# Optimization experiments

Measured on AMD Instinct MI355X. Metric: run time of the kernel, lower is better.

The kernel has to match this reference:

```python
import jax, jax.numpy as jnp
import numpy as np

B, LP, NC, D, E = 8, 1000, 64, 128, 320  # batch, protein len, compound atoms, hid dim, esm dim


def _linear_params(key, din, dout):
    k1, k2 = jax.random.split(key)
    lim = 1.0 / np.sqrt(din)
    W = jax.random.uniform(k1, (din, dout), minval=-lim, maxval=lim, dtype=jnp.float32)
    b = jax.random.uniform(k2, (dout,), minval=-lim, maxval=lim, dtype=jnp.float32)
    return W, b


def setup_inputs() -> dict:
    key = jax.random.key(0)
    ks = jax.random.split(key, 14)
    inp = {
        "protein_embedding": jax.random.normal(ks[0], (B, LP, E), dtype=jnp.float32),
        "protein_feat_x": jax.random.normal(ks[1], (B, LP, D), dtype=jnp.float32),
        "compound_feats": jax.random.normal(ks[2], (B, NC, D), dtype=jnp.float32),
    }
    layers = [("emb", E, D), ("wq", D, D), ("wk", D, D), ("wv", D, D), ("wo", D, D),
              ("jp", D, D), ("jc", D, D),
              ("c1", D, 1024), ("c2", 1024, 1024), ("c3", 1024, 256), ("c4", 256, 1)]
    for i, (name, din, dout) in enumerate(layers):
        W, b = _linear_params(ks[3 + i], din, dout)
        inp[name + "_w"] = W
        inp[name + "_b"] = b
    return inp


def reference(protein_embedding, protein_feat_x, compound_feats,
              emb_w, emb_b, wq_w, wq_b, wk_w, wk_b, wv_w, wv_b, wo_w, wo_b,
              jp_w, jp_b, jc_w, jc_b,
              c1_w, c1_b, c2_w, c2_b, c3_w, c3_b, c4_w, c4_b):
    # protein sequence embedding -> hid dim
    pe = protein_embedding @ emb_w + emb_b                      # [B, LP, D]
    # single-head cross attention: query = seq embedding, key/value = graph feats
    Q = pe @ wq_w + wq_b
    K = protein_feat_x @ wk_w + wk_b
    V = protein_feat_x @ wv_w + wv_b
    scale = jnp.sqrt(jnp.asarray(D, pe.dtype))                  # n_heads=1 -> head_dim=D
    attn = jax.nn.softmax(jnp.einsum('bqd,bkd->bqk', Q, K) / scale, axis=-1)
    protein_feats = jnp.einsum('bqk,bkd->bqd', attn, V) @ wo_w + wo_b  # [B, LP, D]

    # sigmoid bilinear joint attention over (protein residue, compound atom) pairs
    P = jax.nn.relu(protein_feats) @ jp_w + jp_b                # [B, LP, D]
    C = jax.nn.relu(compound_feats) @ jc_w + jc_b               # [B, NC, D]
    A = jax.nn.sigmoid(jnp.einsum('bid,bkd->bik', P, C))        # [B, LP, NC]
    A = A / jnp.sum(A, axis=(1, 2), keepdims=True)

    # tanh outer product (the costly 4D bikj intermediate) then weighted reduction
    cp = jnp.tanh(protein_feats[:, :, None, :] * compound_feats[:, None, :, :])  # [B, LP, NC, D]
    cp_embedding = jnp.einsum('bikd,bik->bd', cp, A)            # [B, D]

    # classifier MLP (dropout is eval-mode identity)
    h = jax.nn.relu(cp_embedding @ c1_w + c1_b)
    h = jax.nn.relu(h @ c2_w + c2_b)
    h = jax.nn.relu(h @ c3_w + c3_b)
    return h @ c4_w + c4_b                                      # [B, 1]
```

## Files before the change

### kernel.cpp

```cpp
#include <hip/hip_runtime.h>
#include <hip/hip_bf16.h>
#include <math.h>

#define LP 1000
#define NCMP 64
#define NSPLIT 4

typedef _Float16 f16;
typedef f16   v8h __attribute__((ext_vector_type(8)));
typedef float v4f __attribute__((ext_vector_type(4)));

__device__ __forceinline__ float rcp_fast(float x) { return __builtin_amdgcn_rcpf(x); }
__device__ __forceinline__ void fsplit(float x, f16& h, f16& l) {
    h = (f16)x; l = (f16)(x - (float)h);
}

__device__ __forceinline__ void gemm_core(float (*Ws)[128], float (*Xt)[36],
                                          const float* X, const float* W, const float* bias,
                                          float* Y, int K, int rowbase, bool relu_in)
{
    const int t  = threadIdx.x;
    const int r0 = (t >> 5) * 4;
    const int c0 = (t & 31) * 4;
    const int xr = t >> 3, xk = (t & 7) << 2;
    const int xrow = rowbase + xr;
    float4 xv = *(const float4*)(X + (long)xrow * K + xk);
    float4 wv[4];
    #pragma unroll
    for (int u = 0; u < 4; ++u) {
        int s = t + u * 256, r = s >> 5, cb = (s & 31) << 2;
        wv[u] = *(const float4*)(W + (long)r * 128 + cb);
    }
    float acc[4][4] = {};
    for (int k0 = 0; k0 < K; k0 += 32) {
        float4 xs = xv;
        if (relu_in) { xs.x = fmaxf(xs.x,0.f); xs.y = fmaxf(xs.y,0.f);
                       xs.z = fmaxf(xs.z,0.f); xs.w = fmaxf(xs.w,0.f); }
        Xt[xk+0][xr] = xs.x; Xt[xk+1][xr] = xs.y; Xt[xk+2][xr] = xs.z; Xt[xk+3][xr] = xs.w;
        #pragma unroll
        for (int u = 0; u < 4; ++u) {
            int s = t + u * 256, r = s >> 5, cb = (s & 31) << 2;
            *(float4*)&Ws[r][cb] = wv[u];
        }
        __syncthreads();
        if (k0 + 32 < K) {
            xv = *(const float4*)(X + (long)xrow * K + k0 + 32 + xk);
            #pragma unroll
            for (int u = 0; u < 4; ++u) {
                int s = t + u * 256, r = s >> 5, cb = (s & 31) << 2;
                wv[u] = *(const float4*)(W + (long)(k0 + 32 + r) * 128 + cb);
            }
        }
        #pragma unroll
        for (int kk = 0; kk < 32; ++kk) {
            float4 w4 = *(const float4*)&Ws[kk][c0];
            float4 x4 = *(const float4*)&Xt[kk][r0];
            acc[0][0] = fmaf(x4.x, w4.x, acc[0][0]); acc[0][1] = fmaf(x4.x, w4.y, acc[0][1]);
            acc[0][2] = fmaf(x4.x, w4.z, acc[0][2]); acc[0][3] = fmaf(x4.x, w4.w, acc[0][3]);
            acc[1][0] = fmaf(x4.y, w4.x, acc[1][0]); acc[1][1] = fmaf(x4.y, w4.y, acc[1][1]);
            acc[1][2] = fmaf(x4.y, w4.z, acc[1][2]); acc[1][3] = fmaf(x4.y, w4.w, acc[1][3]);
            acc[2][0] = fmaf(x4.z, w4.x, acc[2][0]); acc[2][1] = fmaf(x4.z, w4.y, acc[2][1]);
            acc[2][2] = fmaf(x4.z, w4.z, acc[2][2]); acc[2][3] = fmaf(x4.z, w4.w, acc[2][3]);
            acc[3][0] = fmaf(x4.w, w4.x, acc[3][0]); acc[3][1] = fmaf(x4.w, w4.y, acc[3][1]);
            acc[3][2] = fmaf(x4.w, w4.z, acc[3][2]); acc[3][3] = fmaf(x4.w, w4.w, acc[3][3]);
        }
        __syncthreads();
    }
    float4 bv = bias ? *(const float4*)(bias + c0) : make_float4(0.f,0.f,0.f,0.f);
    #pragma unroll
    for (int i = 0; i < 4; ++i) {
        int row = rowbase + r0 + i;
        float4 o;
        o.x = acc[i][0] + bv.x; o.y = acc[i][1] + bv.y;
        o.z = acc[i][2] + bv.z; o.w = acc[i][3] + bv.w;
        *(float4*)(Y + (long)row * 128 + c0) = o;
    }
}

struct H4 { f16 a, b, c, d; };

__device__ __forceinline__ void gemm_core16(float (*Ws)[128], float (*Xt)[36],
                                            const float* X, const float* W, const float* bias,
                                            f16* Yhi, f16* Ylo, int K, int rowbase)
{
    const int t  = threadIdx.x;
    const int r0 = (t >> 5) * 4;
    const int c0 = (t & 31) * 4;
    const int xr = t >> 3, xk = (t & 7) << 2;
    const int xrow = rowbase + xr;
    float4 xv = *(const float4*)(X + (long)xrow * K + xk);
    float4 wv[4];
    #pragma unroll
    for (int u = 0; u < 4; ++u) {
        int s = t + u * 256, r = s >> 5, cb = (s & 31) << 2;
        wv[u] = *(const float4*)(W + (long)r * 128 + cb);
    }
    float acc[4][4] = {};
    for (int k0 = 0; k0 < K; k0 += 32) {
        Xt[xk+0][xr] = xv.x; Xt[xk+1][xr] = xv.y; Xt[xk+2][xr] = xv.z; Xt[xk+3][xr] = xv.w;
        #pragma unroll
        for (int u = 0; u < 4; ++u) {
            int s = t + u * 256, r = s >> 5, cb = (s & 31) << 2;
            *(float4*)&Ws[r][cb] = wv[u];
        }
        __syncthreads();
        if (k0 + 32 < K) {
            xv = *(const float4*)(X + (long)xrow * K + k0 + 32 + xk);
            #pragma unroll
            for (int u = 0; u < 4; ++u) {
                int s = t + u * 256, r = s >> 5, cb = (s & 31) << 2;
                wv[u] = *(const float4*)(W + (long)(k0 + 32 + r) * 128 + cb);
            }
        }
        #pragma unroll
        for (int kk = 0; kk < 32; ++kk) {
            float4 w4 = *(const float4*)&Ws[kk][c0];
            float4 x4 = *(const float4*)&Xt[kk][r0];
            acc[0][0] = fmaf(x4.x, w4.x, acc[0][0]); acc[0][1] = fmaf(x4.x, w4.y, acc[0][1]);
            acc[0][2] = fmaf(x4.x, w4.z, acc[0][2]); acc[0][3] = fmaf(x4.x, w4.w, acc[0][3]);
            acc[1][0] = fmaf(x4.y, w4.x, acc[1][0]); acc[1][1] = fmaf(x4.y, w4.y, acc[1][1]);
            acc[1][2] = fmaf(x4.y, w4.z, acc[1][2]); acc[1][3] = fmaf(x4.y, w4.w, acc[1][3]);
            acc[2][0] = fmaf(x4.z, w4.x, acc[2][0]); acc[2][1] = fmaf(x4.z, w4.y, acc[2][1]);
            acc[2][2] = fmaf(x4.z, w4.z, acc[2][2]); acc[2][3] = fmaf(x4.z, w4.w, acc[2][3]);
            acc[3][0] = fmaf(x4.w, w4.x, acc[3][0]); acc[3][1] = fmaf(x4.w, w4.y, acc[3][1]);
            acc[3][2] = fmaf(x4.w, w4.z, acc[3][2]); acc[3][3] = fmaf(x4.w, w4.w, acc[3][3]);
        }
        __syncthreads();
    }
    float4 bv = *(const float4*)(bias + c0);
    #pragma unroll
    for (int i = 0; i < 4; ++i) {
        int row = rowbase + r0 + i;
        int bb = row / 1000, rr = row - bb * 1000;
        long base = ((long)bb * 1024 + rr) * 128 + c0;
        float o0 = acc[i][0]+bv.x, o1 = acc[i][1]+bv.y, o2 = acc[i][2]+bv.z, o3 = acc[i][3]+bv.w;
        H4 h, l;
        fsplit(o0, h.a, l.a); fsplit(o1, h.b, l.b); fsplit(o2, h.c, l.c); fsplit(o3, h.d, l.d);
        *(H4*)(Yhi + base) = h;
        *(H4*)(Ylo + base) = l;
    }
}

__global__ __launch_bounds__(256) void pre0_k(const float* __restrict__ emb_w, const float* __restrict__ emb_b,
                                              const float* __restrict__ wq_w, const float* __restrict__ wq_b,
                                              const float* __restrict__ wv_w, const float* __restrict__ wv_b,
                                              const float* __restrict__ wo_w, const float* __restrict__ wo_b,
                                              float* __restrict__ Wp, float* __restrict__ bp,
                                              float* __restrict__ Wvo, float* __restrict__ bvo,
                                              float* __restrict__ zbase)
{
    __shared__ __align__(16) float Ws[32][128];
    __shared__ __align__(16) float Xt[32][36];
    const int bid = blockIdx.x;
    if (bid < 10) { gemm_core(Ws, Xt, emb_w, wq_w, nullptr, Wp, 128, bid * 32, false); return; }
    if (bid >= 11 && bid < 15) { gemm_core(Ws, Xt, wv_w, wo_w, nullptr, Wvo, 128, (bid - 11) * 32, false); return; }
    int t = threadIdx.x;
    if (bid == 10 && t >= 128) {
        for (int i = t - 128; i < 1032; i += 128) zbase[i] = 0.f;
        return;
    }
    if (t < 128) {
        const float* vb = (bid == 10) ? emb_b : wv_b;
        const float* Wm = (bid == 10) ? wq_w  : wo_w;
        const float* ab = (bid == 10) ? wq_b  : wo_b;
        float a0 = 0.f, a1 = 0.f, a2 = 0.f, a3 = 0.f;
        for (int k = 0; k < 128; k += 4) {
            a0 = fmaf(vb[k+0], Wm[(k+0)*128 + t], a0);
            a1 = fmaf(vb[k+1], Wm[(k+1)*128 + t], a1);
            a2 = fmaf(vb[k+2], Wm[(k+2)*128 + t], a2);
            a3 = fmaf(vb[k+3], Wm[(k+3)*128 + t], a3);
        }
        float* dst = (bid == 10) ? bp : bvo;
        dst[t] = (a0 + a1) + (a2 + a3) + ab[t];
    }
}

__global__ __launch_bounds__(256) void qkv_k(const float* __restrict__ PE, const float* __restrict__ Wp,
                                             const float* __restrict__ bp, const float* __restrict__ PFX,
                                             const float* __restrict__ wk_w, const float* __restrict__ wk_b,
                                             const float* __restrict__ CF, const float* __restrict__ jc_w,
                                             const float* __restrict__ jc_b,
                                             f16* __restrict__ Qhi, f16* __restrict__ Qlo,
                                             f16* __restrict__ Khi, f16* __restrict__ Klo,
                                             f16* __restrict__ Vthi, f16* __restrict__ Vtlo,
                                             float* __restrict__ Cj)
{
    __shared__ __align__(16) float Ws[32][128];
    __shared__ __align__(16) float Xt[32][36];
    const int bid = blockIdx.x;
    if (bid < 250) { gemm_core16(Ws, Xt, PE, Wp, bp, Qhi, Qlo, 320, bid * 32); return; }
    if (bid < 500) { gemm_core16(Ws, Xt, PFX, wk_w, wk_b, Khi, Klo, 128, (bid - 250) * 32); return; }
    if (bid < 516) { gemm_core(Ws, Xt, CF, jc_w, jc_b, Cj, 128, (bid - 500) * 32, true); return; }
    const int t = threadIdx.x;
    const int rowbase = (bid - 516) * 32;
    const int d = t >> 1, half = t & 1;
    #pragma unroll 4
    for (int i = 0; i < 16; ++i) {
        int row = rowbase + half * 16 + i;
        int bb = row / 1000, rr = row - bb * 1000;
        float v = PFX[(long)row * 128 + d];
        f16 h, l; fsplit(v, h, l);
        long o = ((long)bb * 128 + d) * 1024 + rr;
        Vthi[o] = h; Vtlo[o] = l;
    }
}

__global__ __launch_bounds__(256) void flash7_k(const f16* __restrict__ Qhi, const f16* __restrict__ Qlo,
                                                const f16* __restrict__ Khi, const f16* __restrict__ Klo,
                                                const f16* __restrict__ Vthi, const f16* __restrict__ Vtlo,
                                                float* __restrict__ Opart,
                                                float* __restrict__ mpart, float* __restrict__ lpart)
{
    __shared__ __align__(16) f16 KVhi[9216];
    __shared__ __align__(16) f16 KVlo[9216];
    __shared__ __align__(16) f16 Pshi[4][16 * 72];
    __shared__ __align__(16) f16 Pslo[4][16 * 72];
    const int t    = threadIdx.x;
    const int wv   = t >> 6;
    const int lane = t & 63;
    const int quad = lane >> 4;
    const int l4   = lane & 15;
    const int qt = blockIdx.x, sp = blockIdx.y, b = blockIdx.z;
    const int q0 = qt * 64;
    const float SCALE = 0.08838834764831845f;
    const float L2E   = 1.4426950408889634f;

    int qrow = q0 + wv * 16 + l4; if (qrow >= LP) qrow = LP - 1;
    const long qbase = ((long)b * 1024 + qrow) * 128;
    v8h qh[4], ql[4];
    #pragma unroll
    for (int kt4 = 0; kt4 < 4; ++kt4) {
        qh[kt4] = *(const v8h*)(Qhi + qbase + kt4 * 32 + quad * 8);
        ql[kt4] = *(const v8h*)(Qlo + qbase + kt4 * 32 + quad * 8);
    }
    float m_i[4] = { -3.0e38f, -3.0e38f, -3.0e38f, -3.0e38f };
    float l_i[4] = { 0.f, 0.f, 0.f, 0.f };
    v4f  O[8];
    #pragma unroll
    for (int dt = 0; dt < 8; ++dt) O[dt] = (v4f){0.f, 0.f, 0.f, 0.f};

    for (int kt = sp * 4; kt < sp * 4 + 4; ++kt) {
        const int key0 = kt * 64;
        __syncthreads();
        #pragma unroll
        for (int u = 0; u < 4; ++u) {
            int ch = t + u * 256;
            int r = ch >> 4, co = (ch & 15) * 8;
            long ga = ((long)b * 1024 + key0 + r) * 128 + co;
            *(v8h*)(KVhi + r * 136 + co) = *(const v8h*)(Khi + ga);
            *(v8h*)(KVlo + r * 136 + co) = *(const v8h*)(Klo + ga);
        }
        __syncthreads();
        v8h vh[4], vl[4];
        #pragma unroll
        for (int u = 0; u < 4; ++u) {
            int ch = t + u * 256;
            int d = ch >> 3, co = (ch & 7) * 8;
            long ga = ((long)b * 128 + d) * 1024 + key0 + co;
            vh[u] = *(const v8h*)(Vthi + ga);
            vl[u] = *(const v8h*)(Vtlo + ga);
        }
        v4f S[4];
        #pragma unroll
        for (int nt = 0; nt < 4; ++nt) S[nt] = (v4f){0.f, 0.f, 0.f, 0.f};
        #pragma unroll
        for (int nt = 0; nt < 4; ++nt) {
            const int rb = (nt * 16 + l4) * 136;
            #pragma unroll
            for (int kt4 = 0; kt4 < 4; ++kt4) {
                v8h bh = *(const v8h*)(KVhi + rb + kt4 * 32 + quad * 8);
                v8h bl = *(const v8h*)(KVlo + rb + kt4 * 32 + quad * 8);
                S[nt] = __builtin_amdgcn_mfma_f32_16x16x32_f16(qh[kt4], bh, S[nt], 0, 0, 0);
                S[nt] = __builtin_amdgcn_mfma_f32_16x16x32_f16(qh[kt4], bl, S[nt], 0, 0, 0);
                S[nt] = __builtin_amdgcn_mfma_f32_16x16x32_f16(ql[kt4], bh, S[nt], 0, 0, 0);
            }
        }
        #pragma unroll
        for (int nt = 0; nt < 4; ++nt) {
            bool valid = (key0 + nt * 16 + l4) < LP;
            #pragma unroll
            for (int r = 0; r < 4; ++r)
                S[nt][r] = valid ? S[nt][r] * SCALE : -3.0e38f;
        }
        float alpha[4];
        #pragma unroll
        for (int r = 0; r < 4; ++r) {
            float tm = fmaxf(fmaxf(S[0][r], S[1][r]), fmaxf(S[2][r], S[3][r]));
            tm = fmaxf(tm, __shfl_xor(tm, 1));
            tm = fmaxf(tm, __shfl_xor(tm, 2));
            tm = fmaxf(tm, __shfl_xor(tm, 4));
            tm = fmaxf(tm, __shfl_xor(tm, 8));
            float mnew = fmaxf(m_i[r], tm);
            alpha[r] = exp2f((m_i[r] - mnew) * L2E);
            float ps = 0.f;
            #pragma unroll
            for (int nt = 0; nt < 4; ++nt) {
                float p = exp2f((S[nt][r] - mnew) * L2E);
                S[nt][r] = p;
                ps += p;
            }
            ps += __shfl_xor(ps, 1);
            ps += __shfl_xor(ps, 2);
            ps += __shfl_xor(ps, 4);
            ps += __shfl_xor(ps, 8);
            l_i[r] = l_i[r] * alpha[r] + ps;
            m_i[r] = mnew;
        }
        #pragma unroll
        for (int dt = 0; dt < 8; ++dt) {
            O[dt][0] *= alpha[0]; O[dt][1] *= alpha[1];
            O[dt][2] *= alpha[2]; O[dt][3] *= alpha[3];
        }
        __syncthreads();
        #pragma unroll
        for (int u = 0; u < 4; ++u) {
            int ch = t + u * 256;
            int d = ch >> 3, co = (ch & 7) * 8;
            *(v8h*)(KVhi + d * 72 + co) = vh[u];
            *(v8h*)(KVlo + d * 72 + co) = vl[u];
        }
        #pragma unroll
        for (int nt = 0; nt < 4; ++nt) {
            int col = nt * 16 + l4;
            #pragma unroll
            for (int r = 0; r < 4; ++r) {
                f16 ph, pl; fsplit(S[nt][r], ph, pl);
                Pshi[wv][(quad * 4 + r) * 72 + col] = ph;
                Pslo[wv][(quad * 4 + r) * 72 + col] = pl;
            }
        }
        __syncthreads();
        #pragma unroll
        for (int kc = 0; kc < 2; ++kc) {
            v8h pah = *(const v8h*)(Pshi[wv] + l4 * 72 + kc * 32 + quad * 8);
            v8h pal = *(const v8h*)(Pslo[wv] + l4 * 72 + kc * 32 + quad * 8);
            #pragma unroll
            for (int dt = 0; dt < 8; ++dt) {
                v8h vfh = *(const v8h*)(KVhi + (dt * 16 + l4) * 72 + kc * 32 + quad * 8);
                v8h vfl = *(const v8h*)(KVlo + (dt * 16 + l4) * 72 + kc * 32 + quad * 8);
                O[dt] = __builtin_amdgcn_mfma_f32_16x16x32_f16(pah, vfh, O[dt], 0, 0, 0);
                O[dt] = __builtin_amdgcn_mfma_f32_16x16x32_f16(pah, vfl, O[dt], 0, 0, 0);
                O[dt] = __builtin_amdgcn_mfma_f32_16x16x32_f16(pal, vfh, O[dt], 0, 0, 0);
            }
        }
    }
    #pragma unroll
    for (int r = 0; r < 4; ++r) {
        int row = q0 + wv * 16 + quad * 4 + r;
        if (row < LP) {
            long base = (long)sp * 1024000 + ((long)b * LP + row) * 128;
            #pragma unroll
            for (int dt = 0; dt < 8; ++dt)
                Opart[base + dt * 16 + l4] = O[dt][r];
            if (l4 == 0) {
                mpart[(long)sp * 8000 + b * LP + row] = m_i[r];
                lpart[(long)sp * 8000 + b * LP + row] = l_i[r];
            }
        }
    }
}

__global__ __launch_bounds__(256) void mt1a_k(
    const float* __restrict__ Opart, const float* __restrict__ mp, const float* __restrict__ lp,
    const float* __restrict__ Wvo, const float* __restrict__ bvo, float* __restrict__ PF)
{
    __shared__ __align__(16) float Ws[128][128];
    __shared__ __align__(16) float Xs[16][132];
    const int t  = threadIdx.x;
    const int p0 = blockIdx.x * 16;
    const int b  = blockIdx.y;
    const float L2E = 1.4426950408889634f;

    #pragma unroll
    for (int u = 0; u < 16; ++u) {
        int s = t + u * 256, r = s >> 5, cb = (s & 31) << 2;
        *(float4*)&Ws[r][cb] = *(const float4*)(Wvo + (long)r * 128 + cb);
    }
    {
        const int pr = t >> 4, pc = (t & 15) << 3;
        int grow = p0 + pr; if (grow > LP - 1) grow = LP - 1;
        const long g = (long)b * LP + grow;
        float mm = -3.0e38f;
        #pragma unroll
        for (int s = 0; s < NSPLIT; ++s) mm = fmaxf(mm, mp[g + (long)s * 8000]);
        float wgt[NSPLIT]; float ls = 0.f;
        #pragma unroll
        for (int s = 0; s < NSPLIT; ++s) {
            wgt[s] = exp2f((mp[g + (long)s * 8000] - mm) * L2E);
            ls += wgt[s] * lp[g + (long)s * 8000];
        }
        const float linv = 1.0f / ls;
        float4 a0 = make_float4(0.f,0.f,0.f,0.f), a1 = make_float4(0.f,0.f,0.f,0.f);
        #pragma unroll
        for (int s = 0; s < NSPLIT; ++s) {
            const float* src = Opart + (long)s * 1024000 + g * 128 + pc;
            float4 p = *(const float4*)src;
            float4 q = *(const float4*)(src + 4);
            a0.x = fmaf(wgt[s], p.x, a0.x); a0.y = fmaf(wgt[s], p.y, a0.y);
            a0.z = fmaf(wgt[s], p.z, a0.z); a0.w = fmaf(wgt[s], p.w, a0.w);
            a1.x = fmaf(wgt[s], q.x, a1.x); a1.y = fmaf(wgt[s], q.y, a1.y);
            a1.z = fmaf(wgt[s], q.z, a1.z); a1.w = fmaf(wgt[s], q.w, a1.w);
        }
        *(float4*)&Xs[pr][pc]     = make_float4(a0.x*linv, a0.y*linv, a0.z*linv, a0.w*linv);
        *(float4*)&Xs[pr][pc + 4] = make_float4(a1.x*linv, a1.y*linv, a1.z*linv, a1.w*linv);
    }
    __syncthreads();
    const int r0 = (t >> 5) * 2;
    const int c0 = (t & 31) * 4;
    float acc[2][4] = {};
    #pragma unroll 8
    for (int kk4 = 0; kk4 < 128; kk4 += 4) {
        float4 xa = *(const float4*)&Xs[r0 + 0][kk4];
        float4 xb = *(const float4*)&Xs[r0 + 1][kk4];
        #pragma unroll
        for (int j = 0; j < 4; ++j) {
            float4 w4 = *(const float4*)&Ws[kk4 + j][c0];
            float x0 = (j==0)?xa.x:(j==1)?xa.y:(j==2)?xa.z:xa.w;
            float x1 = (j==0)?xb.x:(j==1)?xb.y:(j==2)?xb.z:xb.w;
            acc[0][0]=fmaf(x0,w4.x,acc[0][0]); acc[0][1]=fmaf(x0,w4.y,acc[0][1]);
            acc[0][2]=fmaf(x0,w4.z,acc[0][2]); acc[0][3]=fmaf(x0,w4.w,acc[0][3]);
            acc[1][0]=fmaf(x1,w4.x,acc[1][0]); acc[1][1]=fmaf(x1,w4.y,acc[1][1]);
            acc[1][2]=fmaf(x1,w4.z,acc[1][2]); acc[1][3]=fmaf(x1,w4.w,acc[1][3]);
        }
    }
    float4 bv = *(const float4*)(bvo + c0);
    #pragma unroll
    for (int i = 0; i < 2; ++i) {
        int orow = p0 + r0 + i;
        if (orow < LP)
            *(float4*)(PF + ((long)b * LP + orow) * 128 + c0) =
                make_float4(acc[i][0]+bv.x, acc[i][1]+bv.y, acc[i][2]+bv.z, acc[i][3]+bv.w);
    }
}

__global__ __launch_bounds__(256) void mt1b_k(
    const float* __restrict__ PF, const float* __restrict__ jp_w, const float* __restrict__ jp_b,
    float* __restrict__ PJ)
{
    __shared__ __align__(16) float Ws[128][128];
    __shared__ __align__(16) float Xs[16][132];
    const int t  = threadIdx.x;
    const int p0 = blockIdx.x * 16;
    const int b  = blockIdx.y;

    #pragma unroll
    for (int u = 0; u < 16; ++u) {
        int s = t + u * 256, r = s >> 5, cb = (s & 31) << 2;
        *(float4*)&Ws[r][cb] = *(const float4*)(jp_w + (long)r * 128 + cb);
    }
    {
        const int pr = t >> 4, pc = (t & 15) << 3;
        int grow = p0 + pr; if (grow > LP - 1) grow = LP - 1;
        const float* src = PF + ((long)b * LP + grow) * 128 + pc;
        float4 p = *(const float4*)src;
        float4 q = *(const float4*)(src + 4);
        *(float4*)&Xs[pr][pc] =
            make_float4(fmaxf(p.x,0.f), fmaxf(p.y,0.f), fmaxf(p.z,0.f), fmaxf(p.w,0.f));
        *(float4*)&Xs[pr][pc + 4] =
            make_float4(fmaxf(q.x,0.f), fmaxf(q.y,0.f), fmaxf(q.z,0.f), fmaxf(q.w,0.f));
    }
    __syncthreads();
    const int r0 = (t >> 5) * 2;
    const int c0 = (t & 31) * 4;
    float acc[2][4] = {};
    #pragma unroll 8
    for (int kk4 = 0; kk4 < 128; kk4 += 4) {
        float4 xa = *(const float4*)&Xs[r0 + 0][kk4];
        float4 xb = *(const float4*)&Xs[r0 + 1][kk4];
        #pragma unroll
        for (int j = 0; j < 4; ++j) {
            float4 w4 = *(const float4*)&Ws[kk4 + j][c0];
            float x0 = (j==0)?xa.x:(j==1)?xa.y:(j==2)?xa.z:xa.w;
            float x1 = (j==0)?xb.x:(j==1)?xb.y:(j==2)?xb.z:xb.w;
            acc[0][0]=fmaf(x0,w4.x,acc[0][0]); acc[0][1]=fmaf(x0,w4.y,acc[0][1]);
            acc[0][2]=fmaf(x0,w4.z,acc[0][2]); acc[0][3]=fmaf(x0,w4.w,acc[0][3]);
            acc[1][0]=fmaf(x1,w4.x,acc[1][0]); acc[1][1]=fmaf(x1,w4.y,acc[1][1]);
            acc[1][2]=fmaf(x1,w4.z,acc[1][2]); acc[1][3]=fmaf(x1,w4.w,acc[1][3]);
        }
    }
    float4 bv = *(const float4*)(jp_b + c0);
    #pragma unroll
    for (int i = 0; i < 2; ++i) {
        int orow = p0 + r0 + i;
        if (orow < LP)
            *(float4*)(PJ + ((long)b * LP + orow) * 128 + c0) =
                make_float4(acc[i][0]+bv.x, acc[i][1]+bv.y, acc[i][2]+bv.z, acc[i][3]+bv.w);
    }
}

template<int IIN>
__device__ __forceinline__ float tanh_chunk(const float (*Cs)[132], const float (*AshT)[20],
                                            const float* areg, int d, int kh)
{
    float accD = 0.f;
    for (int kk = 0; kk < 16; ++kk) {
        const int k = (kh << 4) + kk;
        const float cv = Cs[k][d];
        #pragma unroll
        for (int iq = 0; iq < IIN; iq += 4) {
            float4 a4 = *(const float4*)&AshT[k][iq];
            float e0 = exp2f(areg[iq+0] * cv);
            float e1 = exp2f(areg[iq+1] * cv);
            float e2 = exp2f(areg[iq+2] * cv);
            float e3 = exp2f(areg[iq+3] * cv);
            accD = fmaf(1.f - 2.f * rcp_fast(e0 + 1.f), a4.x, accD);
            accD = fmaf(1.f - 2.f * rcp_fast(e1 + 1.f), a4.y, accD);
            accD = fmaf(1.f - 2.f * rcp_fast(e2 + 1.f), a4.z, accD);
            accD = fmaf(1.f - 2.f * rcp_fast(e3 + 1.f), a4.w, accD);
        }
    }
    return accD;
}

__global__ __launch_bounds__(256) void mt2_k(
    const float* __restrict__ PF, const float* __restrict__ PJ,
    const float* __restrict__ Cj, const float* __restrict__ CF,
    float* __restrict__ Asum, float* __restrict__ cpe)
{
    __shared__ __align__(16) float Pjs[16][132];
    __shared__ __align__(16) float Pfs[16][132];
    __shared__ __align__(16) float Cs[32][132];
    __shared__ __align__(16) float AshT[32][20];
    __shared__ float red[256];
    const int t  = threadIdx.x;
    const int p0 = blockIdx.x * 16;
    const int kc = blockIdx.y;
    const int b  = blockIdx.z;
    const float L2E = 1.4426950408889634f;

    {
        int pr = t >> 4, pc = (t & 15) << 3;
        int gr = p0 + pr; if (gr > LP - 1) gr = LP - 1;
        long gb = ((long)b * LP + gr) * 128 + pc;
        *(float4*)&Pjs[pr][pc]     = *(const float4*)(PJ + gb);
        *(float4*)&Pjs[pr][pc + 4] = *(const float4*)(PJ + gb + 4);
        *(float4*)&Pfs[pr][pc]     = *(const float4*)(PF + gb);
        *(float4*)&Pfs[pr][pc + 4] = *(const float4*)(PF + gb + 4);
    }
    float4 cfv[4];
    #pragma unroll
    for (int u = 0; u < 4; ++u) {
        int s = t + u * 256, r = s >> 5, cb = (s & 31) << 2;
        *(float4*)&Cs[r][cb] = *(const float4*)(Cj + ((long)b * NCMP + kc * 32 + r) * 128 + cb);
        cfv[u] = *(const float4*)(CF + ((long)b * NCMP + kc * 32 + r) * 128 + cb);
    }
    __syncthreads();
    const int tr = t >> 4, tc = t & 15;
    float sacc[2] = {0.f, 0.f};
    #pragma unroll 4
    for (int d4 = 0; d4 < 32; ++d4) {
        float4 p4 = *(const float4*)&Pjs[tr][d4 << 2];
        #pragma unroll
        for (int j = 0; j < 2; ++j) {
            float4 cv = *(const float4*)&Cs[tc + (j << 4)][d4 << 2];
            sacc[j] += p4.x*cv.x + p4.y*cv.y + p4.z*cv.z + p4.w*cv.w;
        }
    }
    float lsum = 0.f;
    const int gi = p0 + tr;
    #pragma unroll
    for (int j = 0; j < 2; ++j) {
        float sg = rcp_fast(1.f + exp2f(-sacc[j] * L2E));
        if (gi < LP) { AshT[tc + (j << 4)][tr] = sg; lsum += sg; }
    }
    #pragma unroll
    for (int off = 1; off < 64; off <<= 1) lsum += __shfl_xor(lsum, off);
    if ((t & 63) == 0) red[t >> 6] = lsum;
    __syncthreads();
    if (t == 0) atomicAdd(Asum + b, (red[0] + red[1]) + (red[2] + red[3]));
    #pragma unroll
    for (int u = 0; u < 4; ++u) {
        int s = t + u * 256, r = s >> 5, cb = (s & 31) << 2;
        *(float4*)&Cs[r][cb] = cfv[u];
    }
    __syncthreads();
    const float TWO_L2E = 2.8853900817779268f;
    const int d = t & 127, kh = t >> 7;
    float areg[16];
    #pragma unroll
    for (int ii = 0; ii < 16; ++ii) areg[ii] = Pfs[ii][d] * TWO_L2E;
    float accD = (p0 + 16 <= LP) ? tanh_chunk<16>(Cs, AshT, areg, d, kh)
                                 : tanh_chunk<8>(Cs, AshT, areg, d, kh);
    red[t] = accD;
    __syncthreads();
    if (t < 128) atomicAdd(cpe + (long)b * 128 + t, red[t] + red[t + 128]);
}

__global__ __launch_bounds__(256) void c12_k(const float* __restrict__ cpe, const float* __restrict__ Asum,
                                             const float* __restrict__ c1_w, const float* __restrict__ c1_b,
                                             const float* __restrict__ c2_w, float* __restrict__ part)
{
    __shared__ float sc[8][128];
    __shared__ float ins[8][8];
    const int t = threadIdx.x, ks = blockIdx.x, k0 = ks * 8;
    #pragma unroll
    for (int u = 0; u < 4; ++u) {
        int idx = t + u * 256;
        sc[idx >> 7][idx & 127] = cpe[idx] * rcp_fast(Asum[idx >> 7]);
    }
    __syncthreads();
    if (t < 64) {
        int b = t >> 3, kk = t & 7;
        int n1 = k0 + kk;
        float a0 = 0.f, a1 = 0.f, a2 = 0.f, a3 = 0.f;
        #pragma unroll 8
        for (int j = 0; j < 128; j += 4) {
            a0 = fmaf(sc[b][j+0], c1_w[(long)(j+0)*1024 + n1], a0);
            a1 = fmaf(sc[b][j+1], c1_w[(long)(j+1)*1024 + n1], a1);
            a2 = fmaf(sc[b][j+2], c1_w[(long)(j+2)*1024 + n1], a2);
            a3 = fmaf(sc[b][j+3], c1_w[(long)(j+3)*1024 + n1], a3);
        }
        ins[b][kk] = fmaxf((a0 + a1) + (a2 + a3) + c1_b[n1], 0.f);
    }
    __syncthreads();
    const int n = (t & 63) * 4 + (t >> 6) * 256;
    float4 acc[8] = {};
    #pragma unroll
    for (int kk = 0; kk < 8; ++kk) {
        float4 w4 = *(const float4*)(c2_w + (long)(k0 + kk) * 1024 + n);
        #pragma unroll
        for (int b = 0; b < 8; ++b) {
            float s = ins[b][kk];
            acc[b].x = fmaf(s, w4.x, acc[b].x); acc[b].y = fmaf(s, w4.y, acc[b].y);
            acc[b].z = fmaf(s, w4.z, acc[b].z); acc[b].w = fmaf(s, w4.w, acc[b].w);
        }
    }
    #pragma unroll
    for (int b = 0; b < 8; ++b)
        *(float4*)(part + ((long)(ks * 8 + b)) * 1024 + n) = acc[b];
}

__global__ __launch_bounds__(256) void c3m_k(const float* __restrict__ part2, const float* __restrict__ c2_b,
                                             const float* __restrict__ c3_w, const float* __restrict__ c3_b,
                                             const float* __restrict__ c4_w, const float* __restrict__ c4_b,
                                             float* __restrict__ out)
{
    __shared__ float Hs[1024];
    __shared__ float red[256];
    const int t = threadIdx.x, b = blockIdx.x;
    float4 acc4 = make_float4(0.f,0.f,0.f,0.f);
    #pragma unroll 4
    for (int ks = 0; ks < 128; ++ks) {
        float4 p = *(const float4*)(part2 + ((long)(ks * 8 + b)) * 1024 + t * 4);
        acc4.x += p.x; acc4.y += p.y; acc4.z += p.z; acc4.w += p.w;
    }
    {
        float4 bb = *(const float4*)(c2_b + t * 4);
        Hs[t*4+0] = fmaxf(acc4.x + bb.x, 0.f);
        Hs[t*4+1] = fmaxf(acc4.y + bb.y, 0.f);
        Hs[t*4+2] = fmaxf(acc4.z + bb.z, 0.f);
        Hs[t*4+3] = fmaxf(acc4.w + bb.w, 0.f);
    }
    __syncthreads();
    float a0 = 0.f, a1 = 0.f, a2 = 0.f, a3 = 0.f;
    #pragma unroll 8
    for (int k = 0; k < 1024; k += 4) {
        a0 = fmaf(Hs[k+0], c3_w[(long)(k+0)*256 + t], a0);
        a1 = fmaf(Hs[k+1], c3_w[(long)(k+1)*256 + t], a1);
        a2 = fmaf(Hs[k+2], c3_w[(long)(k+2)*256 + t], a2);
        a3 = fmaf(Hs[k+3], c3_w[(long)(k+3)*256 + t], a3);
    }
    float h3v = fmaxf((a0 + a1) + (a2 + a3) + c3_b[t], 0.f);
    red[t] = h3v * c4_w[t];
    __syncthreads();
    for (int off = 128; off > 0; off >>= 1) {
        if (t < off) red[t] += red[t + off];
        __syncthreads();
    }
    if (t == 0) out[b] = red[0] + c4_b[0];
}

extern "C" void kernel_launch(void* const* d_in, const int* in_sizes, int n_in,
                              void* d_out, int out_size, void* d_ws, size_t ws_size,
                              hipStream_t stream)
{
    const float* PE   = (const float*)d_in[0];
    const float* PFX  = (const float*)d_in[1];
    const float* CF   = (const float*)d_in[2];
    const float* emb_w = (const float*)d_in[3];  const float* emb_b = (const float*)d_in[4];
    const float* wq_w  = (const float*)d_in[5];  const float* wq_b  = (const float*)d_in[6];
    const float* wk_w  = (const float*)d_in[7];  const float* wk_b  = (const float*)d_in[8];
    const float* wv_w  = (const float*)d_in[9];  const float* wv_b  = (const float*)d_in[10];
    const float* wo_w  = (const float*)d_in[11]; const float* wo_b  = (const float*)d_in[12];
    const float* jp_w  = (const float*)d_in[13]; const float* jp_b  = (const float*)d_in[14];
    const float* jc_w  = (const float*)d_in[15]; const float* jc_b  = (const float*)d_in[16];
    const float* c1_w  = (const float*)d_in[17]; const float* c1_b  = (const float*)d_in[18];
    const float* c2_w  = (const float*)d_in[19]; const float* c2_b  = (const float*)d_in[20];
    const float* c3_w  = (const float*)d_in[21]; const float* c3_b  = (const float*)d_in[22];
    const float* c4_w  = (const float*)d_in[23]; const float* c4_b  = (const float*)d_in[24];

    float* ws     = (float*)d_ws;
    f16*  Qhi   = (f16*)ws;
    f16*  Qlo   = (f16*)(ws + 524288);
    f16*  Khi   = (f16*)(ws + 1048576);
    f16*  Klo   = (f16*)(ws + 1572864);
    f16*  Vthi  = (f16*)(ws + 2097152);
    f16*  Vtlo  = (f16*)(ws + 2621440);
    float* bufC   = ws + 3145728;
    float* Opart  = bufC + 65536;
    float* mpart  = Opart + 4096000;
    float* lpart  = mpart + 32000;
    float* Asum   = lpart + 32000;
    float* cpe    = Asum + 8;
    float* bprime = cpe + 1024;
    float* bufWp  = bprime + 128;
    float* bufWvo = bufWp + 40960;
    float* bufbvo = bufWvo + 16384;
    float* part2  = ws;
    float* PFbuf  = ws + 1048576;
    float* PJbuf  = ws + 2097152;

    pre0_k<<<16, 256, 0, stream>>>(emb_w, emb_b, wq_w, wq_b, wv_w, wv_b, wo_w, wo_b,
                                   bufWp, bprime, bufWvo, bufbvo, Asum);
    qkv_k<<<766, 256, 0, stream>>>(PE, bufWp, bprime, PFX, wk_w, wk_b, CF, jc_w, jc_b,
                                   Qhi, Qlo, Khi, Klo, Vthi, Vtlo, bufC);
    flash7_k<<<dim3(16, NSPLIT, 8), 256, 0, stream>>>(Qhi, Qlo, Khi, Klo, Vthi, Vtlo,
                                                      Opart, mpart, lpart);
    mt1a_k<<<dim3(63, 8), 256, 0, stream>>>(Opart, mpart, lpart, bufWvo, bufbvo, PFbuf);
    mt1b_k<<<dim3(63, 8), 256, 0, stream>>>(PFbuf, jp_w, jp_b, PJbuf);
    mt2_k<<<dim3(63, 2, 8), 256, 0, stream>>>(PFbuf, PJbuf, bufC, CF, Asum, cpe);
    c12_k<<<128, 256, 0, stream>>>(cpe, Asum, c1_w, c1_b, c2_w, part2);
    c3m_k<<<8, 256, 0, stream>>>(part2, c2_b, c3_w, c3_b, c4_w, c4_b, (float*)d_out);
}
```

Before: 274.5 us.

## Compute Q and K projections with split-f16 MFMA instead of FP32 FMA

Replaces the scalar FP32 tiled GEMM for the Q and K projections with MFMA 16x16x32 f16 instructions, using hi/lo f16 splits (three MFMAs per tile) to keep near-FP32 accuracy. A new split kernel first converts the inputs and transposed weights into hi/lo f16 buffers, and the V transpose moves into that kernel. This adds an extra launch and extra global traffic for the split buffers, in exchange for matrix-core throughput. Operands are read straight from global memory without LDS staging.

```diff
diff --git a/kernel.cpp b/kernel.cpp
--- a/kernel.cpp
+++ b/kernel.cpp
@@ -14,6 +14,8 @@
 __device__ __forceinline__ void fsplit(float x, f16& h, f16& l) {
     h = (f16)x; l = (f16)(x - (float)h);
 }
+
+struct H4 { f16 a, b, c, d; };
 
 __device__ __forceinline__ void gemm_core(float (*Ws)[128], float (*Xt)[36],
                                           const float* X, const float* W, const float* bias,
@@ -77,70 +79,6 @@
     }
 }
 
-struct H4 { f16 a, b, c, d; };
-
-__device__ __forceinline__ void gemm_core16(float (*Ws)[128], float (*Xt)[36],
-                                            const float* X, const float* W, const float* bias,
-                                            f16* Yhi, f16* Ylo, int K, int rowbase)
-{
-    const int t  = threadIdx.x;
-    const int r0 = (t >> 5) * 4;
-    const int c0 = (t & 31) * 4;
-    const int xr = t >> 3, xk = (t & 7) << 2;
-    const int xrow = rowbase + xr;
-    float4 xv = *(const float4*)(X + (long)xrow * K + xk);
-    float4 wv[4];
-    #pragma unroll
-    for (int u = 0; u < 4; ++u) {
-        int s = t + u * 256, r = s >> 5, cb = (s & 31) << 2;
-        wv[u] = *(const float4*)(W + (long)r * 128 + cb);
-    }
-    float acc[4][4] = {};
-    for (int k0 = 0; k0 < K; k0 += 32) {
-        Xt[xk+0][xr] = xv.x; Xt[xk+1][xr] = xv.y; Xt[xk+2][xr] = xv.z; Xt[xk+3][xr] = xv.w;
-        #pragma unroll
-        for (int u = 0; u < 4; ++u) {
-            int s = t + u * 256, r = s >> 5, cb = (s & 31) << 2;
-            *(float4*)&Ws[r][cb] = wv[u];
-        }
-        __syncthreads();
-        if (k0 + 32 < K) {
-            xv = *(const float4*)(X + (long)xrow * K + k0 + 32 + xk);
-            #pragma unroll
-            for (int u = 0; u < 4; ++u) {
-                int s = t + u * 256, r = s >> 5, cb = (s & 31) << 2;
-                wv[u] = *(const float4*)(W + (long)(k0 + 32 + r) * 128 + cb);
-            }
-        }
-        #pragma unroll
-        for (int kk = 0; kk < 32; ++kk) {
-            float4 w4 = *(const float4*)&Ws[kk][c0];
-            float4 x4 = *(const float4*)&Xt[kk][r0];
-            acc[0][0] = fmaf(x4.x, w4.x, acc[0][0]); acc[0][1] = fmaf(x4.x, w4.y, acc[0][1]);
-            acc[0][2] = fmaf(x4.x, w4.z, acc[0][2]); acc[0][3] = fmaf(x4.x, w4.w, acc[0][3]);
-            acc[1][0] = fmaf(x4.y, w4.x, acc[1][0]); acc[1][1] = fmaf(x4.y, w4.y, acc[1][1]);
-            acc[1][2] = fmaf(x4.y, w4.z, acc[1][2]); acc[1][3] = fmaf(x4.y, w4.w, acc[1][3]);
-            acc[2][0] = fmaf(x4.z, w4.x, acc[2][0]); acc[2][1] = fmaf(x4.z, w4.y, acc[2][1]);
-            acc[2][2] = fmaf(x4.z, w4.z, acc[2][2]); acc[2][3] = fmaf(x4.z, w4.w, acc[2][3]);
-            acc[3][0] = fmaf(x4.w, w4.x, acc[3][0]); acc[3][1] = fmaf(x4.w, w4.y, acc[3][1]);
-            acc[3][2] = fmaf(x4.w, w4.z, acc[3][2]); acc[3][3] = fmaf(x4.w, w4.w, acc[3][3]);
-        }
-        __syncthreads();
-    }
-    float4 bv = *(const float4*)(bias + c0);
-    #pragma unroll
-    for (int i = 0; i < 4; ++i) {
-        int row = rowbase + r0 + i;
-        int bb = row / 1000, rr = row - bb * 1000;
-        long base = ((long)bb * 1024 + rr) * 128 + c0;
-        float o0 = acc[i][0]+bv.x, o1 = acc[i][1]+bv.y, o2 = acc[i][2]+bv.z, o3 = acc[i][3]+bv.w;
-        H4 h, l;
-        fsplit(o0, h.a, l.a); fsplit(o1, h.b, l.b); fsplit(o2, h.c, l.c); fsplit(o3, h.d, l.d);
-        *(H4*)(Yhi + base) = h;
-        *(H4*)(Ylo + base) = l;
-    }
-}
-
 __global__ __launch_bounds__(256) void pre0_k(const float* __restrict__ emb_w, const float* __restrict__ emb_b,
                                               const float* __restrict__ wq_w, const float* __restrict__ wq_b,
                                               const float* __restrict__ wv_w, const float* __restrict__ wv_b,
@@ -175,33 +113,135 @@
     }
 }
 
-__global__ __launch_bounds__(256) void qkv_k(const float* __restrict__ PE, const float* __restrict__ Wp,
-                                             const float* __restrict__ bp, const float* __restrict__ PFX,
-                                             const float* __restrict__ wk_w, const float* __restrict__ wk_b,
-                                             const float* __restrict__ CF, const float* __restrict__ jc_w,
-                                             const float* __restrict__ jc_b,
-                                             f16* __restrict__ Qhi, f16* __restrict__ Qlo,
-                                             f16* __restrict__ Khi, f16* __restrict__ Klo,
-                                             f16* __restrict__ Vthi, f16* __restrict__ Vtlo,
-                                             float* __restrict__ Cj)
+__global__ __launch_bounds__(256) void split_k(
+    const float* __restrict__ PE, const float* __restrict__ PFX,
+    const float* __restrict__ Wp, const float* __restrict__ wk_w,
+    f16* __restrict__ PEhi, f16* __restrict__ PElo,
+    f16* __restrict__ PXhi, f16* __restrict__ PXlo,
+    f16* __restrict__ Vthi, f16* __restrict__ Vtlo,
+    f16* __restrict__ WpThi, f16* __restrict__ WpTlo,
+    f16* __restrict__ WkThi, f16* __restrict__ WkTlo)
+{
+    const int bid = blockIdx.x, t = threadIdx.x;
+    if (bid < 250) {
+        #pragma unroll
+        for (int u = 0; u < 10; ++u) {
+            int f = t + u * 256, r = f / 80, c = (f - r * 80) * 4;
+            int grow = bid * 32 + r;
+            int bb = grow / 1000, rr = grow - bb * 1000;
+            float4 v = *(const float4*)(PE + (long)grow * 320 + c);
+            H4 h, l;
+            fsplit(v.x, h.a, l.a); fsplit(v.y, h.b, l.b);
+            fsplit(v.z, h.c, l.c); fsplit(v.w, h.d, l.d);
+            long o = ((long)bb * 1024 + rr) * 320 + c;
+            *(H4*)(PEhi + o) = h; *(H4*)(PElo + o) = l;
+        }
+        return;
+    }
+    if (bid < 500) {
+        const int rb = (bid - 250) * 32;
+        #pragma unroll
+        for (int u = 0; u < 4; ++u) {
+            int f = t + u * 256, r = f >> 5, c = (f & 31) * 4;
+            int grow = rb + r;
+            int bb = grow / 1000, rr = grow - bb * 1000;
+            float4 v = *(const float4*)(PFX + (long)grow * 128 + c);
+            H4 h, l;
+            fsplit(v.x, h.a, l.a); fsplit(v.y, h.b, l.b);
+            fsplit(v.z, h.c, l.c); fsplit(v.w, h.d, l.d);
+            long o = ((long)bb * 1024 + rr) * 128 + c;
+            *(H4*)(PXhi + o) = h; *(H4*)(PXlo + o) = l;
+        }
+        const int d = t >> 1, half = t & 1;
+        #pragma unroll 4
+        for (int i = 0; i < 16; ++i) {
+            int row = rb + half * 16 + i;
+            int bb = row / 1000, rr = row - bb * 1000;
+            float v = PFX[(long)row * 128 + d];
+            f16 h, l; fsplit(v, h, l);
+            long o = ((long)bb * 128 + d) * 1024 + rr;
+            Vthi[o] = h; Vtlo[o] = l;
+        }
+        return;
+    }
+    #pragma unroll
+    for (int u = 0; u < 8; ++u) {
+        int idx = (bid - 500) * 2048 + u * 256 + t;
+        if (idx < 40960) {
+            int k = idx >> 7, n = idx & 127;
+            f16 h, l; fsplit(Wp[idx], h, l);
+            WpThi[(long)n * 320 + k] = h; WpTlo[(long)n * 320 + k] = l;
+        } else {
+            int j = idx - 40960;
+            int k = j >> 7, n = j & 127;
+            f16 h, l; fsplit(wk_w[j], h, l);
+            WkThi[(long)n * 128 + k] = h; WkTlo[(long)n * 128 + k] = l;
+        }
+    }
+}
+
+__global__ __launch_bounds__(256) void qkv2_k(
+    const f16* __restrict__ PEhi, const f16* __restrict__ PElo,
+    const f16* __restrict__ PXhi, const f16* __restrict__ PXlo,
+    const f16* __restrict__ WpThi, const f16* __restrict__ WpTlo,
+    const f16* __restrict__ WkThi, const f16* __restrict__ WkTlo,
+    const float* __restrict__ bp, const float* __restrict__ wk_b,
+    const float* __restrict__ CF, const float* __restrict__ jc_w, const float* __restrict__ jc_b,
+    f16* __restrict__ Qhi, f16* __restrict__ Qlo,
+    f16* __restrict__ Khi, f16* __restrict__ Klo,
+    float* __restrict__ Cj)
 {
     __shared__ __align__(16) float Ws[32][128];
     __shared__ __align__(16) float Xt[32][36];
     const int bid = blockIdx.x;
-    if (bid < 250) { gemm_core16(Ws, Xt, PE, Wp, bp, Qhi, Qlo, 320, bid * 32); return; }
-    if (bid < 500) { gemm_core16(Ws, Xt, PFX, wk_w, wk_b, Khi, Klo, 128, (bid - 250) * 32); return; }
-    if (bid < 516) { gemm_core(Ws, Xt, CF, jc_w, jc_b, Cj, 128, (bid - 500) * 32, true); return; }
+    if (bid >= 256) { gemm_core(Ws, Xt, CF, jc_w, jc_b, Cj, 128, (bid - 256) * 32, true); return; }
+    const bool isQ = bid < 128;
+    const int b = (bid & 127) >> 4, tile = bid & 15;
+    const int KD  = isQ ? 320 : 128;
+    const int NCH = isQ ? 10 : 4;
+    const f16* Ahi = isQ ? PEhi : PXhi;
+    const f16* Alo = isQ ? PElo : PXlo;
+    const f16* Bhi = isQ ? WpThi : WkThi;
+    const f16* Blo = isQ ? WpTlo : WkTlo;
+    const float* bias = isQ ? bp : wk_b;
+    f16* Yhi = isQ ? Qhi : Khi;
+    f16* Ylo = isQ ? Qlo : Klo;
+
     const int t = threadIdx.x;
-    const int rowbase = (bid - 516) * 32;
-    const int d = t >> 1, half = t & 1;
-    #pragma unroll 4
-    for (int i = 0; i < 16; ++i) {
-        int row = rowbase + half * 16 + i;
-        int bb = row / 1000, rr = row - bb * 1000;
-        float v = PFX[(long)row * 128 + d];
-        f16 h, l; fsplit(v, h, l);
-        long o = ((long)bb * 128 + d) * 1024 + rr;
-        Vthi[o] = h; Vtlo[o] = l;
+    const int wv = t >> 6, lane = t & 63, quad = lane >> 4, l4 = lane & 15;
+    int arow = tile * 64 + wv * 16 + l4; if (arow >= LP) arow = LP - 1;
+    const f16* ah_p = Ahi + ((long)b * 1024 + arow) * KD;
+    const f16* al_p = Alo + ((long)b * 1024 + arow) * KD;
+
+    v4f acc[8];
+    #pragma unroll
+    for (int dt = 0; dt < 8; ++dt) acc[dt] = (v4f){0.f, 0.f, 0.f, 0.f};
+
+    for (int kt = 0; kt < NCH; ++kt) {
+        const int ko = kt * 32 + quad * 8;
+        v8h ah = *(const v8h*)(ah_p + ko);
+        v8h al = *(const v8h*)(al_p + ko);
+        #pragma unroll
+        for (int dt = 0; dt < 8; ++dt) {
+            const long bo = (long)(dt * 16 + l4) * KD + ko;
+            v8h bh = *(const v8h*)(Bhi + bo);
+            v8h bl = *(const v8h*)(Blo + bo);
+            acc[dt] = __builtin_amdgcn_mfma_f32_16x16x32_f16(ah, bh, acc[dt], 0, 0, 0);
+            acc[dt] = __builtin_amdgcn_mfma_f32_16x16x32_f16(ah, bl, acc[dt], 0, 0, 0);
+            acc[dt] = __builtin_amdgcn_mfma_f32_16x16x32_f16(al, bh, acc[dt], 0, 0, 0);
+        }
+    }
+    #pragma unroll
+    for (int dt = 0; dt < 8; ++dt) {
+        const int col = dt * 16 + l4;
+        const float bv = bias[col];
+        #pragma unroll
+        for (int r = 0; r < 4; ++r) {
+            int row = tile * 64 + wv * 16 + quad * 4 + r;
+            long o = ((long)b * 1024 + row) * 128 + col;
+            f16 h, l; fsplit(acc[dt][r] + bv, h, l);
+            Yhi[o] = h; Ylo[o] = l;
+        }
     }
 }
 
@@ -709,11 +749,24 @@
     float* part2  = ws;
     float* PFbuf  = ws + 1048576;
     float* PJbuf  = ws + 2097152;
+    f16* PEhi  = (f16*)(ws + 7430144);
+    f16* PElo  = (f16*)(ws + 8740864);
+    f16* PXhi  = (f16*)(ws + 10051584);
+    f16* PXlo  = (f16*)(ws + 10575872);
+    f16* WpThi = (f16*)(ws + 11100160);
+    f16* WpTlo = (f16*)(ws + 11120640);
+    f16* WkThi = (f16*)(ws + 11141120);
+    f16* WkTlo = (f16*)(ws + 11149312);
 
     pre0_k<<<16, 256, 0, stream>>>(emb_w, emb_b, wq_w, wq_b, wv_w, wv_b, wo_w, wo_b,
                                    bufWp, bprime, bufWvo, bufbvo, Asum);
-    qkv_k<<<766, 256, 0, stream>>>(PE, bufWp, bprime, PFX, wk_w, wk_b, CF, jc_w, jc_b,
-                                   Qhi, Qlo, Khi, Klo, Vthi, Vtlo, bufC);
+    split_k<<<528, 256, 0, stream>>>(PE, PFX, bufWp, wk_w,
+                                     PEhi, PElo, PXhi, PXlo, Vthi, Vtlo,
+                                     WpThi, WpTlo, WkThi, WkTlo);
+    qkv2_k<<<272, 256, 0, stream>>>(PEhi, PElo, PXhi, PXlo,
+                                    WpThi, WpTlo, WkThi, WkTlo,
+                                    bprime, wk_b, CF, jc_w, jc_b,
+                                    Qhi, Qlo, Khi, Klo, bufC);
     flash7_k<<<dim3(16, NSPLIT, 8), 256, 0, stream>>>(Qhi, Qlo, Khi, Klo, Vthi, Vtlo,
                                                       Opart, mpart, lpart);
     mt1a_k<<<dim3(63, 8), 256, 0, stream>>>(Opart, mpart, lpart, bufWvo, bufbvo, PFbuf);
```

Result: slower. 282.3 us (+2.8%).
